# Performance work log

Hardware: AMD Instinct MI355X
Metric: run time of the kernel (lower is better)

The kernel has to match this reference:

```python
import jax, jax.numpy as jnp
import numpy as np

NT, NGRID, NX = 512, 2048, 16   # time steps, grids/basins, total input features
NY, HID, D = 1, 64, 4           # outputs, hidden size, max delay (lag window)


def setup_inputs() -> dict:
    key = jax.random.key(0)
    ks = jax.random.split(key, 8)
    s_in = 1.0 / np.sqrt(NX).astype(np.float32)
    s_h = 1.0 / np.sqrt(HID).astype(np.float32)
    u = lambda k, shape, s: jax.random.uniform(k, shape, jnp.float32, -s, s)
    return {
        "x": jax.random.normal(ks[0], (NT, NGRID, NX), jnp.float32),
        "W_in": u(ks[1], (NX, HID), s_in),
        "b_in": u(ks[2], (HID,), s_in),
        "W_xh": u(ks[3], (HID, HID), s_h),
        "W_hh": u(ks[4], (HID, HID), s_h),
        "b_h": u(ks[5], (HID,), s_h),
        "W_out": u(ks[6], (HID, NY), s_h),
        "b_out": u(ks[7], (NY,), s_h),
    }


def reference(x, W_in, b_in, W_xh, W_hh, b_h, W_out, b_out):
    nt, ngrid, nx = x.shape
    T = nt - D  # number of predicted steps (t = D .. nt-1)
    # lag-window gather: for output t, window covers x[t-D : t]
    idx = jnp.arange(T)[:, None] + jnp.arange(D)[None, :]  # [T, D]
    exog = x[..., : nx - NY][idx]   # [T, D, ngrid, nx-ny] exogenous inputs
    feed = x[..., nx - NY:][idx]    # [T, D, ngrid, ny]    feedback (observed y)
    win = jnp.concatenate([exog, feed], axis=-1)  # [T, D, ngrid, nx]
    win = jnp.moveaxis(win, 1, 0)                 # [D, T, ngrid, nx] scan over delay

    def step(h, x_d):
        u = jax.nn.relu(x_d @ W_in + b_in)           # linearIn + ReLU
        h_new = jnp.tanh(u @ W_xh + h @ W_hh + b_h)  # Narx (tanh RNN) cell
        return h_new, None

    h0 = jnp.zeros((T, ngrid, HID), x.dtype)
    hT, _ = jax.lax.scan(step, h0, win)   # final hidden state over the window
    yt = hT @ W_out + b_out               # [T, ngrid, ny] linearOut
    out = jnp.zeros((nt, ngrid, NY), x.dtype).at[D:].set(yt)
    return out
```

## Files before the change

kernel.cpp:

```cpp
#include <hip/hip_runtime.h>
#include <hip/hip_bf16.h>


#define NG    2048
#define NXF   16
#define HIDN  64
#define DLAG  4
#define TOUTN 508
#define GBLK  64
#define TTB   4
#define NSLC  (DLAG + TTB - 1)
#define STR   72
#define SW    40
#define SCALE 2.8853900817779268f
#define WXH_OFF 0
#define WHH_OFF 4096
#define BH_OFF  8192

typedef short  s16x8 __attribute__((ext_vector_type(8)));
typedef float  f32x4 __attribute__((ext_vector_type(4)));
typedef unsigned int u32x4 __attribute__((ext_vector_type(4)));

__device__ __forceinline__ unsigned short f2bf(float f) {
    unsigned int u = __float_as_uint(f);
    u += 0x7fffu + ((u >> 16) & 1u);
    return (unsigned short)(u >> 16);
}
__device__ __forceinline__ unsigned int pk2bf(float a, float b) {
    union { __hip_bfloat162 h2; unsigned int u; } c;
    c.h2 = __float22bfloat162_rn(float2{a, b});
    return c.u;
}
__device__ __forceinline__ float raw_exp2(float a) {
#if __has_builtin(__builtin_amdgcn_exp2f)
    return __builtin_amdgcn_exp2f(a);
#else
    float r;
    asm("v_exp_f32 %0, %1" : "=v"(r) : "v"(a));
    return r;
#endif
}
__device__ __forceinline__ float tanh_pre(float a) {
    float e = raw_exp2(a);
    return fmaf(-2.0f, __builtin_amdgcn_rcpf(e + 1.0f), 1.0f);
}

__global__ __launch_bounds__(256, 1)
void pack_weights(const float* __restrict__ Wxh,
                  const float* __restrict__ Whh,
                  const float* __restrict__ bh,
                  unsigned short* __restrict__ ws)
{
    __shared__ unsigned short s_stage[HIDN * STR];
    const int tid  = threadIdx.x;
    const int lane = tid & 63;
    const int lm   = lane & 15;
    const int q    = lane >> 4;
    const int p0   = tid >> 2;
    const int pi0  = 32*(p0>>5) + 16*((p0>>2)&1) + 4*((p0>>3)&3) + (p0&3);
    const int n0   = (tid & 3) * 16;

    if (tid < 64) {
        float* bhs = (float*)(ws + BH_OFF);
        bhs[tid] = bh[tid] * SCALE;
    }

    {
        const float* src = Wxh + pi0 * HIDN + n0;
        #pragma unroll
        for (int i = 0; i < 16; ++i)
            s_stage[(n0 + i) * STR + p0] = f2bf(src[i] * SCALE);
    }
    __syncthreads();
    if (tid < 64) {
        #pragma unroll
        for (int tn = 0; tn < 4; ++tn)
            #pragma unroll
            for (int kk = 0; kk < 2; ++kk)
                *(s16x8*)&ws[WXH_OFF + lane*64 + tn*16 + kk*8] =
                    *(const s16x8*)&s_stage[(tn*16 + lm) * STR + kk*32 + q*8];
    }
    __syncthreads();
    {
        const float* src = Whh + pi0 * HIDN + n0;
        #pragma unroll
        for (int i = 0; i < 16; ++i)
            s_stage[(n0 + i) * STR + p0] = f2bf(src[i] * SCALE);
    }
    __syncthreads();
    if (tid < 64) {
        #pragma unroll
        for (int tn = 0; tn < 4; ++tn)
            #pragma unroll
            for (int kk = 0; kk < 2; ++kk)
                *(s16x8*)&ws[WHH_OFF + lane*64 + tn*16 + kk*8] =
                    *(const s16x8*)&s_stage[(tn*16 + lm) * STR + kk*32 + q*8];
    }
}

__global__ __launch_bounds__(256, 3)
void narx_kernel(const float* __restrict__ x,
                 const float* __restrict__ Win,
                 const float* __restrict__ bin_g,
                 const unsigned short* __restrict__ wfrag,
                 const float* __restrict__ Wout,
                 const float* __restrict__ bout_g,
                 float* __restrict__ out)
{
    __shared__ unsigned short s_win[HIDN * SW];

    const int tid   = threadIdx.x;
    const int lane  = tid & 63;
    const int lm    = lane & 15;
    const int q     = lane >> 4;
    const int G0    = blockIdx.x * GBLK;
    const int tt0   = blockIdx.y * TTB;
    const int wrow0 = (tid >> 6) * 16;
    const int myg   = G0 + wrow0 + lm;

    if (blockIdx.y == 0 && tid < GBLK) {
        #pragma unroll
        for (int t2 = 0; t2 < DLAG; ++t2)
            out[t2 * NG + G0 + tid] = 0.0f;
    }

    s16x8 wxhf[4][2], whhf[4][2];
    #pragma unroll
    for (int tn = 0; tn < 4; ++tn)
        #pragma unroll
        for (int kk = 0; kk < 2; ++kk) {
            wxhf[tn][kk] = *(const s16x8*)&wfrag[WXH_OFF + lane*64 + tn*16 + kk*8];
            whhf[tn][kk] = *(const s16x8*)&wfrag[WHH_OFF + lane*64 + tn*16 + kk*8];
        }
    const float* bhs = (const float*)(wfrag + BH_OFF);

    {
        int r = tid >> 2, c0 = 16 + (tid & 3) * 4;
        #pragma unroll
        for (int i = 0; i < 4; ++i) {
            unsigned short v = 0;
            if (c0 + i == 16) v = f2bf(bin_g[r]);
            s_win[r * SW + c0 + i] = v;
        }
    }
    {
        int k = tid >> 4, nn = (tid & 15) * 4;
        const float* src = Win + k * HIDN + nn;
        #pragma unroll
        for (int i = 0; i < 4; ++i) s_win[(nn + i) * SW + k] = f2bf(src[i]);
    }

    const float boutf = bout_g[0];
    __syncthreads();

    const size_t slcstride = (size_t)NG * NXF;
    const float* px = x + ((size_t)tt0 * NG + myg) * NXF + q * 8;

    auto load_pack = [&](int s) -> s16x8 {
        s16x8 r = {0,0,0,0,0,0,0,0};
        if (q == 2) r[0] = (short)0x3F80;
        if (q < 2) {
            const float* p = px + (size_t)s * slcstride;
            f32x4 a = *(const f32x4*)p;
            f32x4 b = *(const f32x4*)(p + 4);
            u32x4 xi;
            xi[0] = pk2bf(a[0], a[1]);
            xi[1] = pk2bf(a[2], a[3]);
            xi[2] = pk2bf(b[0], b[1]);
            xi[3] = pk2bf(b[2], b[3]);
            r = __builtin_bit_cast(s16x8, xi);
        }
        return r;
    };

    u32x4 hpk[TTB][2];
    s16x8 xf = load_pack(0);

    #pragma unroll
    for (int s = 0; s < NSLC; ++s) {
        s16x8 xf_nxt = xf;
        if (s + 1 < NSLC) xf_nxt = load_pack(s + 1);

        u32x4 upk[2];
        #pragma unroll
        for (int tj = 0; tj < 4; ++tj) {
            s16x8 wf = *(const s16x8*)&s_win[(tj*16 + lm) * SW + q*8];
            f32x4 zc = {0.f, 0.f, 0.f, 0.f};
            f32x4 ua = __builtin_amdgcn_mfma_f32_16x16x32_bf16(wf, xf, zc, 0, 0, 0);
            upk[tj>>1][(tj&1)*2+0] = pk2bf(fmaxf(ua[0],0.f), fmaxf(ua[1],0.f));
            upk[tj>>1][(tj&1)*2+1] = pk2bf(fmaxf(ua[2],0.f), fmaxf(ua[3],0.f));
        }
        const s16x8 uf0 = __builtin_bit_cast(s16x8, upk[0]);
        const s16x8 uf1 = __builtin_bit_cast(s16x8, upk[1]);

        f32x4 axh[4];
        #pragma unroll
        for (int tn = 0; tn < 4; ++tn) {
            f32x4 bh4 = *(const f32x4*)&bhs[tn*16 + q*4];
            axh[tn] = __builtin_amdgcn_mfma_f32_16x16x32_bf16(
                wxhf[tn][0], uf0, bh4, 0, 0, 0);
        }
        #pragma unroll
        for (int tn = 0; tn < 4; ++tn)
            axh[tn] = __builtin_amdgcn_mfma_f32_16x16x32_bf16(
                wxhf[tn][1], uf1, axh[tn], 0, 0, 0);

        #pragma unroll
        for (int ti = 0; ti < TTB; ++ti) {
            if (ti > s || ti < s - (DLAG - 1)) continue;

            f32x4 ha[4];
            if (ti != s) {
                #pragma unroll
                for (int tn = 0; tn < 4; ++tn) {
                    s16x8 hf0 = __builtin_bit_cast(s16x8, hpk[ti][0]);
                    ha[tn] = __builtin_amdgcn_mfma_f32_16x16x32_bf16(
                        whhf[tn][0], hf0, axh[tn], 0, 0, 0);
                }
                #pragma unroll
                for (int tn = 0; tn < 4; ++tn) {
                    s16x8 hf1 = __builtin_bit_cast(s16x8, hpk[ti][1]);
                    ha[tn] = __builtin_amdgcn_mfma_f32_16x16x32_bf16(
                        whhf[tn][1], hf1, ha[tn], 0, 0, 0);
                }
            } else {
                #pragma unroll
                for (int tn = 0; tn < 4; ++tn) ha[tn] = axh[tn];
            }

            if (ti > s - (DLAG - 1)) {
                #pragma unroll
                for (int tn = 0; tn < 4; ++tn) {
                    hpk[ti][tn>>1][(tn&1)*2+0] =
                        pk2bf(tanh_pre(ha[tn][0]), tanh_pre(ha[tn][1]));
                    hpk[ti][tn>>1][(tn&1)*2+1] =
                        pk2bf(tanh_pre(ha[tn][2]), tanh_pre(ha[tn][3]));
                }
            } else {
                float acc = 0.f;
                #pragma unroll
                for (int tn = 0; tn < 4; ++tn) {
                    f32x4 wo = *(const f32x4*)&Wout[tn*16 + q*4];
                    #pragma unroll
                    for (int r = 0; r < 4; ++r)
                        acc += tanh_pre(ha[tn][r]) * wo[r];
                }
                acc += __shfl_xor(acc, 16, 64);
                acc += __shfl_xor(acc, 32, 64);
                if (lane < 16)
                    out[(size_t)(tt0 + ti + DLAG) * NG + G0 + wrow0 + lane] =
                        acc + boutf;
            }
        }

        xf = xf_nxt;
    }
}

extern "C" void kernel_launch(void* const* d_in, const int* in_sizes, int n_in,
                              void* d_out, int out_size, void* d_ws, size_t ws_size,
                              hipStream_t stream) {
    const float* x    = (const float*)d_in[0];
    const float* Win  = (const float*)d_in[1];
    const float* bin  = (const float*)d_in[2];
    const float* Wxh  = (const float*)d_in[3];
    const float* Whh  = (const float*)d_in[4];
    const float* bh   = (const float*)d_in[5];
    const float* Wout = (const float*)d_in[6];
    const float* bout = (const float*)d_in[7];
    float* out = (float*)d_out;
    unsigned short* ws = (unsigned short*)d_ws;

    pack_weights<<<dim3(1), dim3(256), 0, stream>>>(Wxh, Whh, bh, ws);

    dim3 grid(NG / GBLK, TOUTN / TTB);
    narx_kernel<<<grid, dim3(256), 0, stream>>>(x, Win, bin, ws, Wout, bout, out);
}
```

Measured before the change: 207.8 us.

## Stage recurrent weight fragments in LDS instead of registers to raise occupancy

Repacks the bf16 W_xh/W_hh fragments into a lane-contiguous layout and copies them into a 16KB shared buffer per block, reading each fragment from LDS (volatile) right before its MFMA instead of holding 16 fragment vectors in registers. This frees VGPRs, so launch bounds go from 3 to 4 blocks per SIMD-slot to lift occupancy and hide latency. In exchange every MFMA now needs an LDS read inside the hot loop, and the volatile load stops the compiler from hoisting or reusing those reads. Extra shared memory per block may also limit how many blocks fit.

```diff
diff --git a/kernel.cpp b/kernel.cpp
--- a/kernel.cpp
+++ b/kernel.cpp
@@ -44,6 +44,9 @@
     float e = raw_exp2(a);
     return fmaf(-2.0f, __builtin_amdgcn_rcpf(e + 1.0f), 1.0f);
 }
+__device__ __forceinline__ s16x8 lds_frag(const unsigned short* p) {
+    return *(const volatile s16x8*)p;
+}
 
 __global__ __launch_bounds__(256, 1)
 void pack_weights(const float* __restrict__ Wxh,
@@ -77,7 +80,7 @@
         for (int tn = 0; tn < 4; ++tn)
             #pragma unroll
             for (int kk = 0; kk < 2; ++kk)
-                *(s16x8*)&ws[WXH_OFF + lane*64 + tn*16 + kk*8] =
+                *(s16x8*)&ws[WXH_OFF + ((tn*2 + kk)*64 + lane)*8] =
                     *(const s16x8*)&s_stage[(tn*16 + lm) * STR + kk*32 + q*8];
     }
     __syncthreads();
@@ -93,12 +96,12 @@
         for (int tn = 0; tn < 4; ++tn)
             #pragma unroll
             for (int kk = 0; kk < 2; ++kk)
-                *(s16x8*)&ws[WHH_OFF + lane*64 + tn*16 + kk*8] =
+                *(s16x8*)&ws[WHH_OFF + ((tn*2 + kk)*64 + lane)*8] =
                     *(const s16x8*)&s_stage[(tn*16 + lm) * STR + kk*32 + q*8];
     }
 }
 
-__global__ __launch_bounds__(256, 3)
+__global__ __launch_bounds__(256, 4)
 void narx_kernel(const float* __restrict__ x,
                  const float* __restrict__ Win,
                  const float* __restrict__ bin_g,
@@ -108,6 +111,7 @@
                  float* __restrict__ out)
 {
     __shared__ unsigned short s_win[HIDN * SW];
+    __shared__ unsigned short s_wf[8192];
 
     const int tid   = threadIdx.x;
     const int lane  = tid & 63;
@@ -124,14 +128,12 @@
             out[t2 * NG + G0 + tid] = 0.0f;
     }
 
-    s16x8 wxhf[4][2], whhf[4][2];
-    #pragma unroll
-    for (int tn = 0; tn < 4; ++tn)
-        #pragma unroll
-        for (int kk = 0; kk < 2; ++kk) {
-            wxhf[tn][kk] = *(const s16x8*)&wfrag[WXH_OFF + lane*64 + tn*16 + kk*8];
-            whhf[tn][kk] = *(const s16x8*)&wfrag[WHH_OFF + lane*64 + tn*16 + kk*8];
-        }
+    {
+        const s16x8* g = (const s16x8*)(wfrag + tid * 32);
+        s16x8* d = (s16x8*)(s_wf + tid * 32);
+        #pragma unroll
+        for (int i = 0; i < 4; ++i) d[i] = g[i];
+    }
     const float* bhs = (const float*)(wfrag + BH_OFF);
 
     {
@@ -152,6 +154,9 @@
 
     const float boutf = bout_g[0];
     __syncthreads();
+
+    const unsigned short* wxh_base = &s_wf[WXH_OFF + lane*8];
+    const unsigned short* whh_base = &s_wf[WHH_OFF + lane*8];
 
     const size_t slcstride = (size_t)NG * NXF;
     const float* px = x + ((size_t)tt0 * NG + myg) * NXF + q * 8;
@@ -198,12 +203,12 @@
         for (int tn = 0; tn < 4; ++tn) {
             f32x4 bh4 = *(const f32x4*)&bhs[tn*16 + q*4];
             axh[tn] = __builtin_amdgcn_mfma_f32_16x16x32_bf16(
-                wxhf[tn][0], uf0, bh4, 0, 0, 0);
+                lds_frag(wxh_base + (tn*2 + 0)*512), uf0, bh4, 0, 0, 0);
         }
         #pragma unroll
         for (int tn = 0; tn < 4; ++tn)
             axh[tn] = __builtin_amdgcn_mfma_f32_16x16x32_bf16(
-                wxhf[tn][1], uf1, axh[tn], 0, 0, 0);
+                lds_frag(wxh_base + (tn*2 + 1)*512), uf1, axh[tn], 0, 0, 0);
 
         #pragma unroll
         for (int ti = 0; ti < TTB; ++ti) {
@@ -211,18 +216,16 @@
 
             f32x4 ha[4];
             if (ti != s) {
-                #pragma unroll
-                for (int tn = 0; tn < 4; ++tn) {
-                    s16x8 hf0 = __builtin_bit_cast(s16x8, hpk[ti][0]);
+                s16x8 hf0 = __builtin_bit_cast(s16x8, hpk[ti][0]);
+                s16x8 hf1 = __builtin_bit_cast(s16x8, hpk[ti][1]);
+                #pragma unroll
+                for (int tn = 0; tn < 4; ++tn)
                     ha[tn] = __builtin_amdgcn_mfma_f32_16x16x32_bf16(
-                        whhf[tn][0], hf0, axh[tn], 0, 0, 0);
-                }
-                #pragma unroll
-                for (int tn = 0; tn < 4; ++tn) {
-                    s16x8 hf1 = __builtin_bit_cast(s16x8, hpk[ti][1]);
+                        lds_frag(whh_base + (tn*2 + 0)*512), hf0, axh[tn], 0, 0, 0);
+                #pragma unroll
+                for (int tn = 0; tn < 4; ++tn)
                     ha[tn] = __builtin_amdgcn_mfma_f32_16x16x32_bf16(
-                        whhf[tn][1], hf1, ha[tn], 0, 0, 0);
-                }
+                        lds_frag(whh_base + (tn*2 + 1)*512), hf1, ha[tn], 0, 0, 0);
             } else {
                 #pragma unroll
                 for (int tn = 0; tn < 4; ++tn) ha[tn] = axh[tn];
```

After: 222.9 us. 7.3% more time.

## Move W_hh fragments and hidden-state carries to LDS to raise occupancy

Applied to the files above, without the earlier changes.

Stores the W_hh MFMA fragments in a lane-contiguous layout and stages them, the bias and the per-timestep hidden state into shared memory instead of keeping them in registers. This cuts VGPR pressure so launch bounds can request 4 blocks per SIMD instead of 3. In exchange every recurrent MFMA now reads its weight and hidden operands from LDS, adding LDS traffic and latency. The shared memory per block also grows, which may itself limit occupancy.

```diff
diff --git a/kernel.cpp b/kernel.cpp
--- a/kernel.cpp
+++ b/kernel.cpp
@@ -93,12 +93,12 @@
         for (int tn = 0; tn < 4; ++tn)
             #pragma unroll
             for (int kk = 0; kk < 2; ++kk)
-                *(s16x8*)&ws[WHH_OFF + lane*64 + tn*16 + kk*8] =
+                *(s16x8*)&ws[WHH_OFF + ((tn*2 + kk)*64 + lane)*8] =
                     *(const s16x8*)&s_stage[(tn*16 + lm) * STR + kk*32 + q*8];
     }
 }
 
-__global__ __launch_bounds__(256, 3)
+__global__ __launch_bounds__(256, 4)
 void narx_kernel(const float* __restrict__ x,
                  const float* __restrict__ Win,
                  const float* __restrict__ bin_g,
@@ -108,6 +108,9 @@
                  float* __restrict__ out)
 {
     __shared__ unsigned short s_win[HIDN * SW];
+    __shared__ unsigned short s_whh[4096];
+    __shared__ float          s_bh[HIDN];
+    __shared__ u32x4          s_hpk[3][2][256];
 
     const int tid   = threadIdx.x;
     const int lane  = tid & 63;
@@ -124,15 +127,18 @@
             out[t2 * NG + G0 + tid] = 0.0f;
     }
 
-    s16x8 wxhf[4][2], whhf[4][2];
+    s16x8 wxhf[4][2];
     #pragma unroll
     for (int tn = 0; tn < 4; ++tn)
         #pragma unroll
-        for (int kk = 0; kk < 2; ++kk) {
+        for (int kk = 0; kk < 2; ++kk)
             wxhf[tn][kk] = *(const s16x8*)&wfrag[WXH_OFF + lane*64 + tn*16 + kk*8];
-            whhf[tn][kk] = *(const s16x8*)&wfrag[WHH_OFF + lane*64 + tn*16 + kk*8];
-        }
-    const float* bhs = (const float*)(wfrag + BH_OFF);
+
+    #pragma unroll
+    for (int i = 0; i < 2; ++i)
+        *(s16x8*)&s_whh[(tid + i*256)*8] =
+            *(const s16x8*)&wfrag[WHH_OFF + (tid + i*256)*8];
+    if (tid < HIDN) s_bh[tid] = ((const float*)(wfrag + BH_OFF))[tid];
 
     {
         int r = tid >> 2, c0 = 16 + (tid & 3) * 4;
@@ -173,11 +179,12 @@
         return r;
     };
 
-    u32x4 hpk[TTB][2];
     s16x8 xf = load_pack(0);
 
     #pragma unroll
     for (int s = 0; s < NSLC; ++s) {
+        __asm__ __volatile__("" ::: "memory");
+
         s16x8 xf_nxt = xf;
         if (s + 1 < NSLC) xf_nxt = load_pack(s + 1);
 
@@ -196,7 +203,7 @@
         f32x4 axh[4];
         #pragma unroll
         for (int tn = 0; tn < 4; ++tn) {
-            f32x4 bh4 = *(const f32x4*)&bhs[tn*16 + q*4];
+            f32x4 bh4 = *(const f32x4*)&s_bh[tn*16 + q*4];
             axh[tn] = __builtin_amdgcn_mfma_f32_16x16x32_bf16(
                 wxhf[tn][0], uf0, bh4, 0, 0, 0);
         }
@@ -208,34 +215,41 @@
         #pragma unroll
         for (int ti = 0; ti < TTB; ++ti) {
             if (ti > s || ti < s - (DLAG - 1)) continue;
+            const int slot = ti % 3;
 
             f32x4 ha[4];
             if (ti != s) {
-                #pragma unroll
-                for (int tn = 0; tn < 4; ++tn) {
-                    s16x8 hf0 = __builtin_bit_cast(s16x8, hpk[ti][0]);
+                u32x4 h0 = s_hpk[slot][0][tid];
+                u32x4 h1 = s_hpk[slot][1][tid];
+                s16x8 hf0 = __builtin_bit_cast(s16x8, h0);
+                s16x8 hf1 = __builtin_bit_cast(s16x8, h1);
+                #pragma unroll
+                for (int tn = 0; tn < 4; ++tn)
                     ha[tn] = __builtin_amdgcn_mfma_f32_16x16x32_bf16(
-                        whhf[tn][0], hf0, axh[tn], 0, 0, 0);
-                }
-                #pragma unroll
-                for (int tn = 0; tn < 4; ++tn) {
-                    s16x8 hf1 = __builtin_bit_cast(s16x8, hpk[ti][1]);
+                        *(const s16x8*)&s_whh[((tn*2 + 0)*64 + lane)*8],
+                        hf0, axh[tn], 0, 0, 0);
+                #pragma unroll
+                for (int tn = 0; tn < 4; ++tn)
                     ha[tn] = __builtin_amdgcn_mfma_f32_16x16x32_bf16(
-                        whhf[tn][1], hf1, ha[tn], 0, 0, 0);
-                }
+                        *(const s16x8*)&s_whh[((tn*2 + 1)*64 + lane)*8],
+                        hf1, ha[tn], 0, 0, 0);
             } else {
                 #pragma unroll
                 for (int tn = 0; tn < 4; ++tn) ha[tn] = axh[tn];
             }
 
             if (ti > s - (DLAG - 1)) {
-                #pragma unroll
-                for (int tn = 0; tn < 4; ++tn) {
-                    hpk[ti][tn>>1][(tn&1)*2+0] =
-                        pk2bf(tanh_pre(ha[tn][0]), tanh_pre(ha[tn][1]));
-                    hpk[ti][tn>>1][(tn&1)*2+1] =
-                        pk2bf(tanh_pre(ha[tn][2]), tanh_pre(ha[tn][3]));
-                }
+                u32x4 nh0, nh1;
+                nh0[0] = pk2bf(tanh_pre(ha[0][0]), tanh_pre(ha[0][1]));
+                nh0[1] = pk2bf(tanh_pre(ha[0][2]), tanh_pre(ha[0][3]));
+                nh0[2] = pk2bf(tanh_pre(ha[1][0]), tanh_pre(ha[1][1]));
+                nh0[3] = pk2bf(tanh_pre(ha[1][2]), tanh_pre(ha[1][3]));
+                nh1[0] = pk2bf(tanh_pre(ha[2][0]), tanh_pre(ha[2][1]));
+                nh1[1] = pk2bf(tanh_pre(ha[2][2]), tanh_pre(ha[2][3]));
+                nh1[2] = pk2bf(tanh_pre(ha[3][0]), tanh_pre(ha[3][1]));
+                nh1[3] = pk2bf(tanh_pre(ha[3][2]), tanh_pre(ha[3][3]));
+                s_hpk[slot][0][tid] = nh0;
+                s_hpk[slot][1][tid] = nh1;
             } else {
                 float acc = 0.f;
                 #pragma unroll
```

Result: faster. 183.7 us (-11.6%).
